# Kernel optimization log

Hardware: AMD Instinct MI355X
Metric: run time of the kernel (lower is better)

## Reference

```python
import jax, jax.numpy as jnp
import numpy as np

ALPHA = 0.5
TEMPORAL_UNIT = 0
B, T, D = 8, 1024, 320
TIME_MAX = 10_000_000


def setup_inputs() -> dict:
    key = jax.random.key(0)
    k1, k2, k3 = jax.random.split(key, 3)
    z1 = jax.random.normal(k1, (B, T, D), dtype=jnp.float32)
    z2 = jax.random.normal(k2, (B, T, D), dtype=jnp.float32)
    event_time = jnp.sort(
        jax.random.randint(k3, (B, T), 0, TIME_MAX, dtype=jnp.int32), axis=-1
    )
    return {"z1": z1, "z2": z2, "event_time": event_time}


def _neg_logsoftmax_offdiag(sim):
    # tril(sim,-1)[...,:-1] + triu(sim,1)[...,1:]  -> (.., N, N-1), then -log_softmax
    logits = jnp.tril(sim, -1)[..., :-1] + jnp.triu(sim, 1)[..., 1:]
    return -jax.nn.log_softmax(logits, axis=-1)


def _instance_loss(z1, z2):
    b, t = z1.shape[0], z1.shape[1]
    if b == 1:
        return jnp.float32(0.0)
    z = jnp.concatenate([z1, z2], axis=0).transpose(1, 0, 2)  # (T, 2B, D)
    sim = jnp.einsum('tid,tjd->tij', z, z)                    # (T, 2B, 2B)
    logits = _neg_logsoftmax_offdiag(sim)                     # (T, 2B, 2B-1)
    i = jnp.arange(b)
    return (logits[:, i, b + i - 1].mean() + logits[:, b + i, i].mean()) / 2


def _temporal_loss(z1, z2):
    t = z1.shape[1]
    if t == 1:
        return jnp.float32(0.0)
    z = jnp.concatenate([z1, z2], axis=1)                     # (B, 2T, D)
    sim = jnp.einsum('bid,bjd->bij', z, z)                    # (B, 2T, 2T)
    logits = _neg_logsoftmax_offdiag(sim)                     # (B, 2T, 2T-1)
    ti = jnp.arange(t)
    return (logits[:, ti, t + ti - 1].mean() + logits[:, t + ti, ti].mean()) / 2


def _pool_and_filter(z, time):
    # max_pool1d(kernel=2, stride=1) over time axis
    bsz, seq_len, dim = z.shape
    pooled = jnp.maximum(z[:, :-1], z[:, 1:])                  # (B, T-1, D)
    pooled_time = (time[:, :-1] + time[:, 1:]) // 2            # (B, T-1)
    deltas = jnp.diff(time, axis=-1)                           # (B, T-1)
    indices = jnp.argsort(deltas, axis=-1)                     # permutation of 0..T-2
    mask = indices < seq_len // 2                              # exactly T//2 Trues/row
    tm1 = seq_len - 1
    ar = jnp.arange(tm1)
    # stable in-order selection of masked positions: masked keys keep their index,
    # unmasked keys are pushed past the end; sort + take first T//2
    sel = jnp.sort(jnp.where(mask, ar, ar + tm1), axis=-1)[:, : seq_len // 2]
    pooled = jnp.take_along_axis(pooled, sel[:, :, None], axis=1)
    pooled_time = jnp.take_along_axis(pooled_time, sel, axis=1)
    return pooled, pooled_time


def _hier_loss(z1, z2, time, alpha=ALPHA, temporal_unit=TEMPORAL_UNIT):
    loss = jnp.float32(0.0)
    d = 0
    while z1.shape[1] > 1:  # static Python loop over hierarchy levels
        if alpha != 0:
            loss = loss + alpha * _instance_loss(z1, z2)
        if d >= temporal_unit and (1 - alpha) != 0:
            loss = loss + (1 - alpha) * _temporal_loss(z1, z2)
        d += 1
        z1, _ = _pool_and_filter(z1, time)
        z2, time = _pool_and_filter(z2, time)
    if z1.shape[1] == 1:
        if alpha != 0:
            loss = loss + alpha * _instance_loss(z1, z2)
        d += 1
    return loss / d


def reference(z1, z2, event_time):
    return _hier_loss(z1, z2, event_time)
```

## Files before the change

kernel.cpp:

```cpp
#include <hip/hip_runtime.h>
#include <cstdint>
#include <cstddef>

#define D_DIM 320
#define NEGINF (-1e30f)

typedef __attribute__((ext_vector_type(8))) short bf16x8_t;
typedef __attribute__((ext_vector_type(4))) float f32x4_t;
typedef __attribute__((ext_vector_type(16))) float f32x16_t;

struct Tab {
  int T[11], S[11], zoff[11], wsoff[11];
  int tileStart[12], instStart[12], rstart[12];
  float scale[11];
  int totTemp, totInst, totr;
};

__device__ __forceinline__ float bf2f(unsigned short u) {
  union { unsigned int i; float f; } v; v.i = ((unsigned int)u) << 16; return v.f;
}
__device__ __forceinline__ unsigned short f2bf(float f) {
  union { float f; unsigned int i; } u; u.f = f;
  unsigned int b = u.i + 0x7FFFu + ((u.i >> 16) & 1u);
  return (unsigned short)(b >> 16);
}

__device__ __forceinline__ const unsigned short* zrowb(
    const unsigned short* __restrict__ z1, const unsigned short* __restrict__ z2,
    int b, int T, int r) {
  return (r < T) ? (z1 + ((size_t)b * T + r) * D_DIM)
                 : (z2 + ((size_t)b * T + (r - T)) * D_DIM);
}

#define GLOAD_LDS16(SRC, DST)                                                   \
  __builtin_amdgcn_global_load_lds(                                             \
      (const __attribute__((address_space(1))) void*)(SRC),                     \
      (__attribute__((address_space(3))) void*)(DST), 16, 0, 0)

#define BUF1 8192
#define BUF2 16384

#define STAGE(koff, bufofs)                                                     \
    do {                                                                        \
      GLOAD_LDS16(gA0 + (koff), dA0 + (bufofs));                                \
      GLOAD_LDS16(gA1 + (koff), dA1 + (bufofs));                                \
      GLOAD_LDS16(gB0 + (koff), dB0 + (bufofs));                                \
      GLOAD_LDS16(gB1 + (koff), dB1 + (bufofs));                                \
    } while (0)

#define PHASE3(k, bo, bo2, VM, DO_PF)                                           \
    do {                                                                        \
      asm volatile("s_waitcnt vmcnt(" #VM ")" ::: "memory");                    \
      __builtin_amdgcn_s_barrier();                                             \
      if (DO_PF) STAGE((k + 2) * 32, bo2);                                      \
      bf16x8_t af[4], bfr[4];                                                   \
      _Pragma("unroll")                                                         \
      for (int at = 0; at < 4; ++at)                                            \
        af[at] = *(const bf16x8_t*)(vA + (bo) + at * 128);                      \
      _Pragma("unroll")                                                         \
      for (int ct = 0; ct < 4; ++ct)                                            \
        bfr[ct] = *(const bf16x8_t*)(vB + (bo) + ct * 128);                     \
      asm volatile("s_waitcnt lgkmcnt(0)" ::: "memory");                        \
      __builtin_amdgcn_sched_barrier(0);                                        \
      __builtin_amdgcn_s_setprio(1);                                            \
      _Pragma("unroll")                                                         \
      for (int ct = 0; ct < 4; ++ct)                                            \
        _Pragma("unroll")                                                       \
        for (int at = 0; at < 4; ++at)                                          \
          acc[at][ct] = __builtin_amdgcn_mfma_f32_16x16x32_bf16(                \
              af[at], bfr[ct], acc[at][ct], 0, 0, 0);                           \
      __builtin_amdgcn_s_setprio(0);                                            \
    } while (0)

__device__ __forceinline__ void tile_body(
    unsigned char* smem, int tid,
    const unsigned short* zz1, const unsigned short* zz2,
    int b, int T, int S, int rb, int sg,
    float* wm, float* wv) {
  int N = 2 * T;
  int row0 = rb * 128, col0 = sg * 128;
  int w = tid >> 6, lane = tid & 63;
  int lq = lane >> 4, lr = lane & 15;
  int wr = w >> 1, wc = w & 1;

  unsigned short* lds = (unsigned short*)smem;

  int ra0 = row0 + lane;        if (ra0 > N - 1) ra0 = N - 1;
  int ra1 = row0 + 64 + lane;   if (ra1 > N - 1) ra1 = N - 1;
  int ca0 = col0 + lane;        if (ca0 > N - 1) ca0 = N - 1;
  int ca1 = col0 + 64 + lane;   if (ca1 > N - 1) ca1 = N - 1;
  const unsigned short* gA0 = zrowb(zz1, zz2, b, T, ra0) + w * 8;
  const unsigned short* gA1 = zrowb(zz1, zz2, b, T, ra1) + w * 8;
  const unsigned short* gB0 = zrowb(zz1, zz2, b, T, ca0) + w * 8;
  const unsigned short* gB1 = zrowb(zz1, zz2, b, T, ca1) + w * 8;
  unsigned short* dA0 = &lds[((w) * 128 + lane) * 8];
  unsigned short* dA1 = &lds[((w) * 128 + 64 + lane) * 8];
  unsigned short* dB0 = &lds[((4 + w) * 128 + lane) * 8];
  unsigned short* dB1 = &lds[((4 + w) * 128 + 64 + lane) * 8];

  f32x4_t acc[4][4];
#pragma unroll
  for (int at = 0; at < 4; ++at)
#pragma unroll
    for (int ct = 0; ct < 4; ++ct) acc[at][ct] = (f32x4_t)(0.f);

  const unsigned short* vA = &lds[((lq) * 128 + wr * 64 + lr) * 8];
  const unsigned short* vB = &lds[((4 + lq) * 128 + wc * 64 + lr) * 8];

  STAGE(0, 0);
  STAGE(32, BUF1);
  PHASE3(0, 0,    BUF2, 4, 1);
  PHASE3(1, BUF1, 0,    4, 1);
  PHASE3(2, BUF2, BUF1, 4, 1);
  PHASE3(3, 0,    BUF2, 4, 1);
  PHASE3(4, BUF1, 0,    4, 1);
  PHASE3(5, BUF2, BUF1, 4, 1);
  PHASE3(6, 0,    BUF2, 4, 1);
  PHASE3(7, BUF1, 0,    4, 1);
  PHASE3(8, BUF2, 0,    4, 0);
  PHASE3(9, 0,    0,    0, 0);
  __builtin_amdgcn_s_barrier();

  float (*mS)[128] = (float(*)[128])(smem);
  float (*sS)[128] = (float(*)[128])(smem + 1024);
  float (*mC)[128] = (float(*)[128])(smem + 2048);
  float (*sC)[128] = (float(*)[128])(smem + 3072);

#pragma unroll
  for (int at = 0; at < 4; ++at) {
#pragma unroll
    for (int rg = 0; rg < 4; ++rg) {
      int rloc = wr * 64 + at * 16 + lq * 4 + rg;
      int rglob = row0 + rloc;
      float v[4];
#pragma unroll
      for (int ct = 0; ct < 4; ++ct) {
        int cg = col0 + wc * 64 + ct * 16 + lr;
        v[ct] = (cg < N && cg != rglob) ? acc[at][ct][rg] : NEGINF;
      }
      float m = fmaxf(fmaxf(v[0], v[1]), fmaxf(v[2], v[3]));
#pragma unroll
      for (int o = 1; o < 16; o <<= 1) m = fmaxf(m, __shfl_xor(m, o));
      float sv = __expf(v[0] - m) + __expf(v[1] - m) +
                 __expf(v[2] - m) + __expf(v[3] - m);
#pragma unroll
      for (int o = 1; o < 16; o <<= 1) sv += __shfl_xor(sv, o);
      if (lr == 0) { mS[wc][rloc] = m; sS[wc][rloc] = sv; }
    }
  }
  if (rb != sg) {
#pragma unroll
    for (int ct = 0; ct < 4; ++ct) {
      float m = NEGINF;
#pragma unroll
      for (int at = 0; at < 4; ++at)
#pragma unroll
        for (int rg = 0; rg < 4; ++rg) m = fmaxf(m, acc[at][ct][rg]);
      m = fmaxf(m, __shfl_xor(m, 16));
      m = fmaxf(m, __shfl_xor(m, 32));
      float s = 0.f;
#pragma unroll
      for (int at = 0; at < 4; ++at)
#pragma unroll
        for (int rg = 0; rg < 4; ++rg) s += __expf(acc[at][ct][rg] - m);
      s += __shfl_xor(s, 16);
      s += __shfl_xor(s, 32);
      if (lq == 0) {
        mC[wr][wc * 64 + ct * 16 + lr] = m;
        sC[wr][wc * 64 + ct * 16 + lr] = s;
      }
    }
  }
  __syncthreads();

  if (tid < 128) {
    int rglob = row0 + tid;
    if (rglob < N) {
      float m0 = mS[0][tid], m1 = mS[1][tid];
      float m = fmaxf(m0, m1);
      float sv = sS[0][tid] * __expf(m0 - m) + sS[1][tid] * __expf(m1 - m);
      int idx = (b * S + sg) * N + rglob;
      wm[idx] = m;
      wv[idx] = sv;
    }
    if (rb != sg) {
      float m0 = mC[0][tid], m1 = mC[1][tid];
      float m = fmaxf(m0, m1);
      float sv = sC[0][tid] * __expf(m0 - m) + sC[1][tid] * __expf(m1 - m);
      int idx = (b * S + rb) * N + col0 + tid;
      wm[idx] = m;
      wv[idx] = sv;
    }
  }
}

__device__ __forceinline__ float inst_wave(
    const unsigned short* zz1, const unsigned short* zz2, int T, int t, int lane) {
  int lq = lane >> 4, lr = lane & 15;
  const unsigned short* zr = (lr < 8)
      ? zz1 + ((size_t)lr * T + t) * D_DIM
      : zz2 + ((size_t)(lr - 8) * T + t) * D_DIM;
  zr += lq * 8;
  f32x4_t c = (f32x4_t)(0.f);
#pragma unroll
  for (int k = 0; k < 10; ++k) {
    bf16x8_t a = *(const bf16x8_t*)(zr + k * 32);
    c = __builtin_amdgcn_mfma_f32_16x16x32_bf16(a, a, c, 0, 0, 0);
  }
  float lsum = 0.f;
#pragma unroll
  for (int rg = 0; rg < 4; ++rg) {
    int rrow = lq * 4 + rg;
    float v = c[rg];
    float x = (lr != rrow) ? v : NEGINF;
    float m = x;
#pragma unroll
    for (int o = 1; o < 16; o <<= 1) m = fmaxf(m, __shfl_xor(m, o));
    float s = __expf(x - m);
#pragma unroll
    for (int o = 1; o < 16; o <<= 1) s += __shfl_xor(s, o);
    int pos = (rrow < 8) ? rrow + 8 : rrow - 8;
    if (lr == pos) lsum += m + __logf(s) - v;
  }
#pragma unroll
  for (int o = 1; o < 64; o <<= 1) lsum += __shfl_xor(lsum, o);
  return lsum;
}

__global__ __launch_bounds__(256) void convert_kernel(
    const float* __restrict__ i1, const float* __restrict__ i2,
    unsigned short* __restrict__ o1, unsigned short* __restrict__ o2,
    int n4, float* __restrict__ out, int outn) {
  int i = blockIdx.x * 256 + threadIdx.x;
  if (i < outn) out[i] = 0.f;
  int stride = gridDim.x * 256;
  for (int j = i; j < n4; j += stride) {
    float4 v = ((const float4*)i1)[j];
    ushort4 r;
    r.x = f2bf(v.x); r.y = f2bf(v.y); r.z = f2bf(v.z); r.w = f2bf(v.w);
    ((ushort4*)o1)[j] = r;
    float4 u = ((const float4*)i2)[j];
    ushort4 q;
    q.x = f2bf(u.x); q.y = f2bf(u.y); q.z = f2bf(u.z); q.w = f2bf(u.w);
    ((ushort4*)o2)[j] = q;
  }
}

__global__ __launch_bounds__(256, 3) void work0_kernel(
    const int* __restrict__ time0,
    const unsigned short* __restrict__ z1, const unsigned short* __restrict__ z2,
    float* __restrict__ wsm, float* __restrict__ wss,
    float* __restrict__ wsInst,
    int* __restrict__ SET0, int* __restrict__ L0LEN,
    int* __restrict__ SET5, int* __restrict__ L5LEN) {
  __shared__ __align__(16) unsigned char smem[49152];
  int bx = blockIdx.x;
  int tid = threadIdx.x;

  if (bx < 8) {
    int b = bx;
    int lane = tid & 63, wid = tid >> 6;
    int* tcur = (int*)smem;
    unsigned* hist = (unsigned*)(smem + 4096);
    unsigned* cum = (unsigned*)(smem + 8192);
    unsigned long long* arr = (unsigned long long*)(smem + 12288);
    int* sortedIdx = (int*)(smem + 20480);
    int* tnew = (int*)(smem + 24576);
    int* srcK = (int*)(smem + 26624);
    int* setA = (int*)(smem + 28672);
    int* setB = (int*)(smem + 32768);
    int* lenA = (int*)(smem + 36864);
    int* lenB = (int*)(smem + 40960);
    unsigned* minW = (unsigned*)(smem + 43008);
    unsigned* maxW = (unsigned*)(smem + 43072);
    unsigned* wsum = (unsigned*)(smem + 43136);
    int* wcnt = (int*)(smem + 43200);

#pragma unroll
    for (int i = 0; i < 4; ++i) {
      int e = tid + 256 * i;
      tcur[e] = time0[b * 1024 + e];
      setA[e] = e;
      lenA[e] = 1;
    }
    __syncthreads();

    int pp = 0;
    for (int lvl = 1; lvl <= 10; ++lvl) {
      int T = 2048 >> lvl;
      int n = T - 1, half = T >> 1;
      bool act[4];
      int dd[4];
      unsigned bkey[4];
      unsigned mn = 0xFFFFFFFFu, mx = 0u;
#pragma unroll
      for (int i = 0; i < 4; ++i) {
        int e = tid + 256 * i;
        act[i] = e < n;
        dd[i] = 0; bkey[i] = 0;
        if (act[i]) {
          dd[i] = tcur[e + 1] - tcur[e];
          bkey[i] = __float_as_uint((float)dd[i]);
          mn = mn < bkey[i] ? mn : bkey[i];
          mx = mx > bkey[i] ? mx : bkey[i];
        }
        hist[e] = 0;
      }
#pragma unroll
      for (int o = 1; o < 64; o <<= 1) {
        unsigned m2 = (unsigned)__shfl_xor((int)mn, o);
        unsigned x2 = (unsigned)__shfl_xor((int)mx, o);
        mn = mn < m2 ? mn : m2;
        mx = mx > x2 ? mx : x2;
      }
      if (lane == 0) { minW[wid] = mn; maxW[wid] = mx; }
      __syncthreads();

      unsigned bmin = 0xFFFFFFFFu, bmax = 0;
#pragma unroll
      for (int i = 0; i < 4; ++i) {
        bmin = bmin < minW[i] ? bmin : minW[i];
        bmax = bmax > maxW[i] ? bmax : maxW[i];
      }
      unsigned long long range = (unsigned long long)(bmax - bmin) + 1;
      unsigned long long scl = (1024ULL << 30) / range;
      int bkt[4]; unsigned av[4];
#pragma unroll
      for (int i = 0; i < 4; ++i) {
        if (act[i]) {
          int bk = (int)(((unsigned long long)(bkey[i] - bmin) * scl) >> 30);
          bkt[i] = bk > 1023 ? 1023 : bk;
          av[i] = atomicAdd(&hist[bkt[i]], 1u);
        }
      }
      __syncthreads();

      {
        unsigned l0 = hist[4 * tid], l1 = hist[4 * tid + 1],
                 l2 = hist[4 * tid + 2], l3 = hist[4 * tid + 3];
        unsigned s = l0 + l1 + l2 + l3;
        unsigned inc = s;
#pragma unroll
        for (int o = 1; o < 64; o <<= 1) {
          unsigned t = (unsigned)__shfl_up((int)inc, o);
          if (lane >= o) inc += t;
        }
        if (lane == 63) wsum[wid] = inc;
        __syncthreads();
        unsigned wpre = 0;
        for (int j = 0; j < wid; ++j) wpre += wsum[j];
        unsigned ex = wpre + inc - s;
        cum[4 * tid] = ex;
        cum[4 * tid + 1] = ex + l0;
        cum[4 * tid + 2] = ex + l0 + l1;
        cum[4 * tid + 3] = ex + l0 + l1 + l2;
      }
      __syncthreads();

      unsigned long long key[4];
      int base[4], occ[4];
#pragma unroll
      for (int i = 0; i < 4; ++i) {
        base[i] = 0; occ[i] = 0;
        if (act[i]) {
          key[i] = ((unsigned long long)(unsigned)dd[i] << 10) |
                   (unsigned)(tid + 256 * i);
          base[i] = (int)cum[bkt[i]];
          arr[base[i] + av[i]] = key[i];
        }
      }
      __syncthreads();

      int cnt[4] = {0, 0, 0, 0};
      int mocc = 0;
#pragma unroll
      for (int i = 0; i < 4; ++i) {
        if (act[i]) {
          occ[i] = (int)hist[bkt[i]];
          mocc = occ[i] > mocc ? occ[i] : mocc;
        }
      }
      for (int j = 0; j < mocc; ++j) {
#pragma unroll
        for (int i = 0; i < 4; ++i)
          if (j < occ[i]) cnt[i] += (arr[base[i] + j] < key[i]) ? 1 : 0;
      }
#pragma unroll
      for (int i = 0; i < 4; ++i)
        if (act[i]) sortedIdx[base[i] + cnt[i]] = tid + 256 * i;
      __syncthreads();

      bool msk[4]; int rw[4];
#pragma unroll
      for (int i = 0; i < 4; ++i) {
        int k = tid + 256 * i;
        msk[i] = (k < n) && (sortedIdx[k] < half);
        unsigned long long bal = __ballot(msk[i]);
        rw[i] = __popcll(bal & ((1ull << lane) - 1ull));
        if (lane == 0) wcnt[i * 4 + wid] = (int)__popcll(bal);
      }
      __syncthreads();
#pragma unroll
      for (int i = 0; i < 4; ++i) {
        if (msk[i]) {
          int seg = i * 4 + wid;
          int pre = 0;
          for (int j = 0; j < seg; ++j) pre += wcnt[j];
          int rr = pre + rw[i];
          int k = tid + 256 * i;
          srcK[rr] = k;
          tnew[rr] = (tcur[k] + tcur[k + 1]) >> 1;
        }
      }
      __syncthreads();

      if (lvl == 6) {
        int* sp = pp ? setB : setA;
        int* lp = pp ? lenB : lenA;
        if (tid < 32) { sp[tid] = tid; lp[tid] = 1; }
        __syncthreads();
      }
      {
        int ll = (lvl <= 5) ? lvl : (lvl - 5);
        int* sp = pp ? setB : setA;
        int* lp = pp ? lenB : lenA;
        int* sc = pp ? setA : setB;
        int* lc = pp ? lenA : lenB;
        int *gset, *glen;
        if (lvl <= 5) {
          gset = SET0 + b * 5120 + (lvl - 1) * 1024;
          glen = L0LEN + b * 992 + (1024 - (1024 >> (lvl - 1)));
        } else {
          gset = SET5 + b * 160 + (lvl - 6) * 32;
          glen = L5LEN + b * 32 + (32 - (32 >> (lvl - 6)));
        }
        int tmax = half << ll;
#pragma unroll
        for (int i = 0; i < 4; ++i) {
          int s = tid + 256 * i;
          if (s < tmax) {
            int j = s >> ll, e2 = s & ((1 << ll) - 1);
            int k = srcK[j];
            int la = lp[k], lb2 = lp[k + 1];
            int v = -1;
            int sh = ll - 1;
            if (e2 < la) v = sp[(k << sh) + e2];
            else if (e2 < la + lb2) v = sp[((k + 1) << sh) + (e2 - la)];
            if (e2 == 0) { lc[j] = la + lb2; glen[j] = la + lb2; }
            if (v >= 0) { sc[s] = v; gset[s] = v; }
          }
        }
        __syncthreads();
        pp ^= 1;
      }
#pragma unroll
      for (int i = 0; i < 4; ++i) {
        int j = tid + 256 * i;
        if (j < half) tcur[j] = tnew[j];
      }
      __syncthreads();
    }
  } else if (bx < 8 + 1088) {
    const int T = 1024, S = 16;
    int local = bx - 8;
    int b = local % 8;
    int pr = local / 8;
    int rb = 0, tt = pr;
    while (tt >= S - rb) { tt -= S - rb; ++rb; }
    int sg = rb + tt;
    tile_body(smem, tid, z1, z2, b, T, S, rb, sg, wsm, wss);
  } else {
    int iw = (bx - 1096) * 4 + (tid >> 6);
    float lsum = inst_wave(z1, z2, 1024, iw, tid & 63);
    if ((tid & 63) == 0) wsInst[iw] = lsum * (1.0f / 360448.0f);
  }
}

__global__ __launch_bounds__(256) void mat1_kernel(
    unsigned short* __restrict__ z1, unsigned short* __restrict__ z2,
    const int* __restrict__ SET0, const int* __restrict__ L0LEN) {
  int g = blockIdx.x * 256 + threadIdx.x;
  int c = g % 40;
  int t2 = g / 40;
  int rr = t2 % 992;
  int bzi = t2 / 992;
  int b = bzi & 7;
  unsigned short* z = (bzi >> 3) ? z2 : z1;
  int l, j, off0;
  if (rr < 512)      { l = 1; j = rr;       off0 = 0; }
  else if (rr < 768) { l = 2; j = rr - 512; off0 = 512; }
  else if (rr < 896) { l = 3; j = rr - 768; off0 = 768; }
  else if (rr < 960) { l = 4; j = rr - 896; off0 = 896; }
  else               { l = 5; j = rr - 960; off0 = 960; }
  int len = L0LEN[b * 992 + off0 + j];
  const int* st = SET0 + b * 5120 + (l - 1) * 1024 + (j << l);
  const unsigned short* src = z + (size_t)b * 1024 * D_DIM;
  int cc = c * 8;
  bf16x8_t mx = *(const bf16x8_t*)(src + (size_t)st[0] * D_DIM + cc);
  for (int e = 1; e < len; ++e) {
    bf16x8_t a = *(const bf16x8_t*)(src + (size_t)st[e] * D_DIM + cc);
#pragma unroll
    for (int q = 0; q < 8; ++q)
      mx[q] = (bf2f((unsigned short)mx[q]) >= bf2f((unsigned short)a[q])) ? mx[q] : a[q];
  }
  size_t zo = (size_t)2560 * (2048 - (2048 >> l));
  int Tl = 1024 >> l;
  *(bf16x8_t*)(z + zo + ((size_t)b * Tl + j) * D_DIM + cc) = mx;
}

__global__ __launch_bounds__(256, 3) void work45_kernel(
    unsigned short* __restrict__ z1, unsigned short* __restrict__ z2,
    const int* __restrict__ SET5, const int* __restrict__ L5LEN,
    float* __restrict__ wsm, float* __restrict__ wss,
    float* __restrict__ wsInst, Tab tab) {
  __shared__ __align__(16) unsigned char smem[49152];
  int bx = blockIdx.x;
  int tid = threadIdx.x;

  if (bx < 408) {
    int g = tab.tileStart[1] + bx;
    int l = 1;
    while (g >= tab.tileStart[l + 1]) ++l;
    int T = tab.T[l], S = tab.S[l];
    int local = g - tab.tileStart[l];
    int npl = (S * (S + 1)) >> 1;
    int nid = (local % 8) * npl + local / 8;
    int b = nid / npl;
    int pr = nid % npl;
    int rb = 0, tt = pr;
    while (tt >= S - rb) { tt -= S - rb; ++rb; }
    int sg = rb + tt;
    tile_body(smem, tid, z1 + tab.zoff[l], z2 + tab.zoff[l], b, T, S, rb, sg,
              wsm + tab.wsoff[l], wss + tab.wsoff[l]);
  } else if (bx < 486) {
    int g = (bx - 408) * 256 + tid;
    if (g >= 2 * 8 * 31 * 40) return;
    int c = g % 40;
    int t2 = g / 40;
    int rr = t2 % 31;
    int bzi = t2 / 31;
    int b = bzi & 7;
    unsigned short* z = (bzi >> 3) ? z2 : z1;
    int l, j, off5;
    if (rr < 16)      { l = 6;  j = rr;      off5 = 0; }
    else if (rr < 24) { l = 7;  j = rr - 16; off5 = 16; }
    else if (rr < 28) { l = 8;  j = rr - 24; off5 = 24; }
    else if (rr < 30) { l = 9;  j = rr - 28; off5 = 28; }
    else              { l = 10; j = rr - 30; off5 = 30; }
    int len = L5LEN[b * 32 + off5 + j];
    const int* st = SET5 + b * 160 + (l - 6) * 32 + (j << (l - 5));
    const unsigned short* src = z + (size_t)2560 * (2048 - 64) + (size_t)b * 32 * D_DIM;
    int cc = c * 8;
    bf16x8_t mx = *(const bf16x8_t*)(src + (size_t)st[0] * D_DIM + cc);
    for (int e = 1; e < len; ++e) {
      bf16x8_t a = *(const bf16x8_t*)(src + (size_t)st[e] * D_DIM + cc);
#pragma unroll
      for (int q = 0; q < 8; ++q)
        mx[q] = (bf2f((unsigned short)mx[q]) >= bf2f((unsigned short)a[q])) ? mx[q] : a[q];
    }
    size_t zo = (size_t)2560 * (2048 - (2048 >> l));
    int Tl = 1024 >> l;
    *(bf16x8_t*)(z + zo + ((size_t)b * Tl + j) * D_DIM + cc) = mx;
  } else {
    int iw = 1024 + (bx - 486) * 4 + (tid >> 6);
    if (iw < 2016) {
      int l = 1;
      while (iw >= tab.instStart[l + 1]) ++l;
      int t = iw - tab.instStart[l];
      float lsum = inst_wave(z1 + tab.zoff[l], z2 + tab.zoff[l], tab.T[l], t,
                             tid & 63);
      if ((tid & 63) == 0) wsInst[iw] = lsum * tab.scale[l];
    }
  }
}

__global__ __launch_bounds__(256) void final_kernel(
    const unsigned short* __restrict__ z1, const unsigned short* __restrict__ z2,
    const float* __restrict__ wsm, const float* __restrict__ wss,
    const float* __restrict__ wsInst, float* __restrict__ out, Tab tab,
    int nc) {
  int bx = blockIdx.x;
  int tid = threadIdx.x;

  if (bx < nc) {
    int g = bx * 256 + tid;
    float loss = 0.f;
    if (g < tab.totr) {
      int l = 0;
      while (g >= tab.rstart[l + 1]) ++l;
      int row = g - tab.rstart[l];
      int T = tab.T[l], N = 2 * T, S = tab.S[l];
      int b = row / N, r = row % N;
      const float* wm = wsm + tab.wsoff[l];
      const float* wv = wss + tab.wsoff[l];
      float m = NEGINF;
      for (int s = 0; s < S; ++s) m = fmaxf(m, wm[(b * S + s) * N + r]);
      float sv = 0.f;
      for (int s = 0; s < S; ++s) {
        int idx = (b * S + s) * N + r;
        sv += wv[idx] * __expf(wm[idx] - m);
      }
      const unsigned short* zz1 = z1 + tab.zoff[l];
      const unsigned short* zz2 = z2 + tab.zoff[l];
      int pos = (r < T) ? r + T : r - T;
      const bf16x8_t* za = (const bf16x8_t*)zrowb(zz1, zz2, b, T, r);
      const bf16x8_t* zp = (const bf16x8_t*)zrowb(zz1, zz2, b, T, pos);
      float dot = 0.f;
      for (int k = 0; k < D_DIM / 8; ++k) {
        bf16x8_t a = za[k], p = zp[k];
#pragma unroll
        for (int e = 0; e < 8; ++e)
          dot += bf2f((unsigned short)a[e]) * bf2f((unsigned short)p[e]);
      }
      loss = (m + logf(sv) - dot) * tab.scale[l];
    } else if (g < tab.totr + 2016) {
      loss = wsInst[g - tab.totr];
    }
    float v = loss;
#pragma unroll
    for (int o = 1; o < 64; o <<= 1) v += __shfl_xor(v, o);
    __shared__ float part[4];
    int w = tid >> 6;
    if ((tid & 63) == 0) part[w] = v;
    __syncthreads();
    if (tid == 0)
      atomicAdd(out, part[0] + part[1] + part[2] + part[3]);
  } else if (bx < nc + 8) {
    int widx = (bx - nc) * 4 + (tid >> 6);
    int l = 6 + (widx >> 3), b = widx & 7;
    int T = tab.T[l], N = 2 * T;
    const unsigned short* zz1 = z1 + tab.zoff[l];
    const unsigned short* zz2 = z2 + tab.zoff[l];
    int lane = tid & 63;
    int col = lane & 31, h = lane >> 5;
    int rl = (col < N) ? col : 0;
    const unsigned short* rowp = (rl < T)
        ? zz1 + ((size_t)b * T + rl) * D_DIM
        : zz2 + ((size_t)b * T + (rl - T)) * D_DIM;
    rowp += h * 8;
    f32x16_t acc = (f32x16_t)(0.f);
#pragma unroll
    for (int m2 = 0; m2 < 20; ++m2) {
      bf16x8_t a = *(const bf16x8_t*)(rowp + m2 * 16);
      acc = __builtin_amdgcn_mfma_f32_32x32x16_bf16(a, a, acc, 0, 0, 0);
    }
    float lsum = 0.f;
#pragma unroll
    for (int rg = 0; rg < 16; ++rg) {
      int row = (rg & 3) + 8 * (rg >> 2) + 4 * h;
      float x = acc[rg];
      float xm = (col < N && row < N && col != row) ? x : NEGINF;
      float m = xm;
#pragma unroll
      for (int o = 1; o < 32; o <<= 1) m = fmaxf(m, __shfl_xor(m, o));
      float s = __expf(xm - m);
#pragma unroll
      for (int o = 1; o < 32; o <<= 1) s += __shfl_xor(s, o);
      int pos = (row < T) ? row + T : row - T;
      if (row < N && col == pos) lsum += m + __logf(s) - x;
    }
#pragma unroll
    for (int o = 1; o < 64; o <<= 1) lsum += __shfl_xor(lsum, o);
    if (lane == 0) atomicAdd(out, lsum * tab.scale[l]);
  } else {
    int widx = (bx - nc - 8) * 4 + (tid >> 6);
    if (widx < 31) {
      int iw = 2016 + widx;
      int l = 6;
      while (iw >= tab.instStart[l + 1]) ++l;
      int t = iw - tab.instStart[l];
      float lsum = inst_wave(z1 + tab.zoff[l], z2 + tab.zoff[l], tab.T[l], t,
                             tid & 63);
      if ((tid & 63) == 0) atomicAdd(out, lsum * tab.scale[l]);
    }
  }
}

extern "C" void kernel_launch(void* const* d_in, const int* in_sizes, int n_in,
                              void* d_out, int out_size, void* d_ws, size_t ws_size,
                              hipStream_t stream) {
  const float* z1_in = (const float*)d_in[0];
  const float* z2_in = (const float*)d_in[1];
  const int* time_in = (const int*)d_in[2];
  float* out = (float*)d_out;

  Tab tab;
  int zo = 0, wso = 0, ts = 0, is = 0, rs = 0;
  for (int l = 0; l < 11; ++l) {
    int T = 1024 >> l, N = 2 * T;
    int S = (N >= 128) ? N / 128 : 1;
    tab.T[l] = T;
    tab.S[l] = S;
    tab.zoff[l] = zo;
    tab.scale[l] = 1.0f / (352.0f * (float)T);
    tab.tileStart[l] = ts;
    tab.instStart[l] = is;
    tab.wsoff[l] = (T > 1) ? wso : 0;
    tab.rstart[l] = rs;
    if (T > 1) {
      ts += 8 * ((S * (S + 1)) >> 1);
      wso += 8 * S * N;
      if (l <= 5) rs += 8 * N;
    }
    is += T;
    zo += 8 * T * D_DIM;
  }
  tab.tileStart[11] = ts;
  tab.instStart[11] = is;
  for (int l = 6; l <= 11; ++l) tab.rstart[l] = rs;
  tab.totTemp = ts;
  tab.totInst = is;
  tab.totr = rs;

  char* w = (char*)d_ws;
  unsigned short* z1s = (unsigned short*)w; w += (size_t)zo * 2;
  unsigned short* z2s = (unsigned short*)w; w += (size_t)zo * 2;
  float* wsm = (float*)w; w += (size_t)wso * sizeof(float);
  float* wss = (float*)w; w += (size_t)wso * sizeof(float);
  float* wsInst = (float*)w; w += (size_t)is * sizeof(float);
  int* SET0 = (int*)w; w += (size_t)8 * 5120 * sizeof(int);
  int* L0LEN = (int*)w; w += (size_t)8 * 992 * sizeof(int);
  int* SET5 = (int*)w; w += (size_t)8 * 160 * sizeof(int);
  int* L5LEN = (int*)w; w += (size_t)8 * 32 * sizeof(int);

  int n0 = 8 * 1024 * D_DIM;
  convert_kernel<<<2048, 256, 0, stream>>>(z1_in, z2_in, z1s, z2s, n0 / 4,
                                           out, out_size);
  work0_kernel<<<8 + 1088 + 256, 256, 0, stream>>>(
      time_in, z1s, z2s, wsm, wss, wsInst, SET0, L0LEN, SET5, L5LEN);
  mat1_kernel<<<2480, 256, 0, stream>>>(z1s, z2s, SET0, L0LEN);
  work45_kernel<<<408 + 78 + 248, 256, 0, stream>>>(
      z1s, z2s, SET5, L5LEN, wsm, wss, wsInst, tab);
  int nc = (tab.totr + 2016 + 255) / 256;
  final_kernel<<<nc + 16, 256, 0, stream>>>(z1s, z2s, wsm, wss, wsInst, out,
                                            tab, nc);
}
```

Baseline: 117.2 us.

## Capture positive-pair logits in GEMM tiles and widen histogram buckets

```diff
diff --git a/kernel.cpp b/kernel.cpp
--- a/kernel.cpp
+++ b/kernel.cpp
@@ -76,7 +76,7 @@
     unsigned char* smem, int tid,
     const unsigned short* zz1, const unsigned short* zz2,
     int b, int T, int S, int rb, int sg,
-    float* wm, float* wv) {
+    float* wm, float* wv, float* wp) {
   int N = 2 * T;
   int row0 = rb * 128, col0 = sg * 128;
   int w = tid >> 6, lane = tid & 63;
@@ -132,11 +132,17 @@
     for (int rg = 0; rg < 4; ++rg) {
       int rloc = wr * 64 + at * 16 + lq * 4 + rg;
       int rglob = row0 + rloc;
+      int posr = (rglob < T) ? rglob + T : rglob - T;
       float v[4];
 #pragma unroll
       for (int ct = 0; ct < 4; ++ct) {
         int cg = col0 + wc * 64 + ct * 16 + lr;
-        v[ct] = (cg < N && cg != rglob) ? acc[at][ct][rg] : NEGINF;
+        float val = acc[at][ct][rg];
+        if (rglob < N && cg == posr) {
+          wp[b * N + rglob] = val;
+          wp[b * N + cg] = val;
+        }
+        v[ct] = (cg < N && cg != rglob) ? val : NEGINF;
       }
       float m = fmaxf(fmaxf(v[0], v[1]), fmaxf(v[2], v[3]));
 #pragma unroll
@@ -249,7 +255,7 @@
 __global__ __launch_bounds__(256, 3) void work0_kernel(
     const int* __restrict__ time0,
     const unsigned short* __restrict__ z1, const unsigned short* __restrict__ z2,
-    float* __restrict__ wsm, float* __restrict__ wss,
+    float* __restrict__ wsm, float* __restrict__ wss, float* __restrict__ wpos,
     float* __restrict__ wsInst,
     int* __restrict__ SET0, int* __restrict__ L0LEN,
     int* __restrict__ SET5, int* __restrict__ L5LEN) {
@@ -262,19 +268,19 @@
     int lane = tid & 63, wid = tid >> 6;
     int* tcur = (int*)smem;
     unsigned* hist = (unsigned*)(smem + 4096);
-    unsigned* cum = (unsigned*)(smem + 8192);
-    unsigned long long* arr = (unsigned long long*)(smem + 12288);
-    int* sortedIdx = (int*)(smem + 20480);
-    int* tnew = (int*)(smem + 24576);
-    int* srcK = (int*)(smem + 26624);
-    int* setA = (int*)(smem + 28672);
-    int* setB = (int*)(smem + 32768);
-    int* lenA = (int*)(smem + 36864);
-    int* lenB = (int*)(smem + 40960);
-    unsigned* minW = (unsigned*)(smem + 43008);
-    unsigned* maxW = (unsigned*)(smem + 43072);
-    unsigned* wsum = (unsigned*)(smem + 43136);
-    int* wcnt = (int*)(smem + 43200);
+    unsigned short* cum = (unsigned short*)(smem + 12288);
+    unsigned long long* arr = (unsigned long long*)(smem + 16384);
+    int* sortedIdx = (int*)(smem + 24576);
+    int* tnew = (int*)(smem + 28672);
+    int* srcK = (int*)(smem + 30720);
+    int* setA = (int*)(smem + 32768);
+    int* setB = (int*)(smem + 36864);
+    int* lenA = (int*)(smem + 40960);
+    int* lenB = (int*)(smem + 45056);
+    unsigned* minW = (unsigned*)(smem + 47104);
+    unsigned* maxW = (unsigned*)(smem + 47168);
+    unsigned* wsum = (unsigned*)(smem + 47232);
+    int* wcnt = (int*)(smem + 47296);
 
 #pragma unroll
     for (int i = 0; i < 4; ++i) {
@@ -305,6 +311,7 @@
           mx = mx > bkey[i] ? mx : bkey[i];
         }
         hist[e] = 0;
+        hist[e + 1024] = 0;
       }
 #pragma unroll
       for (int o = 1; o < 64; o <<= 1) {
@@ -323,22 +330,23 @@
         bmax = bmax > maxW[i] ? bmax : maxW[i];
       }
       unsigned long long range = (unsigned long long)(bmax - bmin) + 1;
-      unsigned long long scl = (1024ULL << 30) / range;
+      unsigned long long scl = (2048ULL << 30) / range;
       int bkt[4]; unsigned av[4];
 #pragma unroll
       for (int i = 0; i < 4; ++i) {
         if (act[i]) {
           int bk = (int)(((unsigned long long)(bkey[i] - bmin) * scl) >> 30);
-          bkt[i] = bk > 1023 ? 1023 : bk;
+          bkt[i] = bk > 2047 ? 2047 : bk;
           av[i] = atomicAdd(&hist[bkt[i]], 1u);
         }
       }
       __syncthreads();
 
       {
-        unsigned l0 = hist[4 * tid], l1 = hist[4 * tid + 1],
-                 l2 = hist[4 * tid + 2], l3 = hist[4 * tid + 3];
-        unsigned s = l0 + l1 + l2 + l3;
+        unsigned lv[8];
+        unsigned s = 0;
+#pragma unroll
+        for (int j = 0; j < 8; ++j) { lv[j] = hist[8 * tid + j]; s += lv[j]; }
         unsigned inc = s;
 #pragma unroll
         for (int o = 1; o < 64; o <<= 1) {
@@ -350,10 +358,8 @@
         unsigned wpre = 0;
         for (int j = 0; j < wid; ++j) wpre += wsum[j];
         unsigned ex = wpre + inc - s;
-        cum[4 * tid] = ex;
-        cum[4 * tid + 1] = ex + l0;
-        cum[4 * tid + 2] = ex + l0 + l1;
-        cum[4 * tid + 3] = ex + l0 + l1 + l2;
+#pragma unroll
+        for (int j = 0; j < 8; ++j) { cum[8 * tid + j] = (unsigned short)ex; ex += lv[j]; }
       }
       __syncthreads();
 
@@ -468,7 +474,7 @@
     int rb = 0, tt = pr;
     while (tt >= S - rb) { tt -= S - rb; ++rb; }
     int sg = rb + tt;
-    tile_body(smem, tid, z1, z2, b, T, S, rb, sg, wsm, wss);
+    tile_body(smem, tid, z1, z2, b, T, S, rb, sg, wsm, wss, wpos);
   } else {
     int iw = (bx - 1096) * 4 + (tid >> 6);
     float lsum = inst_wave(z1, z2, 1024, iw, tid & 63);
@@ -511,7 +517,7 @@
 __global__ __launch_bounds__(256, 3) void work45_kernel(
     unsigned short* __restrict__ z1, unsigned short* __restrict__ z2,
     const int* __restrict__ SET5, const int* __restrict__ L5LEN,
-    float* __restrict__ wsm, float* __restrict__ wss,
+    float* __restrict__ wsm, float* __restrict__ wss, float* __restrict__ wpos,
     float* __restrict__ wsInst, Tab tab) {
   __shared__ __align__(16) unsigned char smem[49152];
   int bx = blockIdx.x;
@@ -531,7 +537,7 @@
     while (tt >= S - rb) { tt -= S - rb; ++rb; }
     int sg = rb + tt;
     tile_body(smem, tid, z1 + tab.zoff[l], z2 + tab.zoff[l], b, T, S, rb, sg,
-              wsm + tab.wsoff[l], wss + tab.wsoff[l]);
+              wsm + tab.wsoff[l], wss + tab.wsoff[l], wpos + tab.rstart[l]);
   } else if (bx < 486) {
     int g = (bx - 408) * 256 + tid;
     if (g >= 2 * 8 * 31 * 40) return;
@@ -577,6 +583,7 @@
 __global__ __launch_bounds__(256) void final_kernel(
     const unsigned short* __restrict__ z1, const unsigned short* __restrict__ z2,
     const float* __restrict__ wsm, const float* __restrict__ wss,
+    const float* __restrict__ wpos,
     const float* __restrict__ wsInst, float* __restrict__ out, Tab tab,
     int nc) {
   int bx = blockIdx.x;
@@ -600,18 +607,7 @@
         int idx = (b * S + s) * N + r;
         sv += wv[idx] * __expf(wm[idx] - m);
       }
-      const unsigned short* zz1 = z1 + tab.zoff[l];
-      const unsigned short* zz2 = z2 + tab.zoff[l];
-      int pos = (r < T) ? r + T : r - T;
-      const bf16x8_t* za = (const bf16x8_t*)zrowb(zz1, zz2, b, T, r);
-      const bf16x8_t* zp = (const bf16x8_t*)zrowb(zz1, zz2, b, T, pos);
-      float dot = 0.f;
-      for (int k = 0; k < D_DIM / 8; ++k) {
-        bf16x8_t a = za[k], p = zp[k];
-#pragma unroll
-        for (int e = 0; e < 8; ++e)
-          dot += bf2f((unsigned short)a[e]) * bf2f((unsigned short)p[e]);
-      }
+      float dot = wpos[tab.rstart[l] + b * N + r];
       loss = (m + logf(sv) - dot) * tab.scale[l];
     } else if (g < tab.totr + 2016) {
       loss = wsInst[g - tab.totr];
@@ -717,6 +713,7 @@
   unsigned short* z2s = (unsigned short*)w; w += (size_t)zo * 2;
   float* wsm = (float*)w; w += (size_t)wso * sizeof(float);
   float* wss = (float*)w; w += (size_t)wso * sizeof(float);
+  float* wpos = (float*)w; w += (size_t)rs * sizeof(float);
   float* wsInst = (float*)w; w += (size_t)is * sizeof(float);
   int* SET0 = (int*)w; w += (size_t)8 * 5120 * sizeof(int);
   int* L0LEN = (int*)w; w += (size_t)8 * 992 * sizeof(int);
@@ -727,11 +724,11 @@
   convert_kernel<<<2048, 256, 0, stream>>>(z1_in, z2_in, z1s, z2s, n0 / 4,
                                            out, out_size);
   work0_kernel<<<8 + 1088 + 256, 256, 0, stream>>>(
-      time_in, z1s, z2s, wsm, wss, wsInst, SET0, L0LEN, SET5, L5LEN);
+      time_in, z1s, z2s, wsm, wss, wpos, wsInst, SET0, L0LEN, SET5, L5LEN);
   mat1_kernel<<<2480, 256, 0, stream>>>(z1s, z2s, SET0, L0LEN);
   work45_kernel<<<408 + 78 + 248, 256, 0, stream>>>(
-      z1s, z2s, SET5, L5LEN, wsm, wss, wsInst, tab);
+      z1s, z2s, SET5, L5LEN, wsm, wss, wpos, wsInst, tab);
   int nc = (tab.totr + 2016 + 255) / 256;
-  final_kernel<<<nc + 16, 256, 0, stream>>>(z1s, z2s, wsm, wss, wsInst, out,
-                                            tab, nc);
-}
+  final_kernel<<<nc + 16, 256, 0, stream>>>(z1s, z2s, wsm, wss, wpos, wsInst,
+                                            out, tab, nc);
+}
```

Result: faster. 104.0 us (-11.2%).
